# Kernel tuning notes

Measured on AMD Instinct MI355X. Metric: run time of the kernel, lower is better.

Reference implementation:

```python
import jax, jax.numpy as jnp
import numpy as np

C = 384        # channels
T_KERNEL = 121 # self.t, temporal kernel support
T_SIM = 65536  # simulated samples
SIZE = 2       # batch of simulations
BLOCK = 512    # overlap-add FFT block size (fast length >= T_KERNEL)


def _oa_conv_dewhiten(noise, spatial_std, vt_spatial, kernel_fft, s2):
    """Overlap-add FFT filtering (single_inv_oaconv1d, norm='ortho') then
    spatial dewhitening einsum, as in StationaryFactorizedNoise.simulate."""
    N, t_padded = noise.shape
    block_size = 2 * (kernel_fft.shape[0] - 1)
    t_out = t_padded - s2 + 1              # valid-conv output length
    hop = block_size - s2 + 1              # overlap-add segment length
    nb = -(-t_padded // hop)               # ceil division
    pad = nb * hop - t_padded
    x = jnp.pad(noise, ((0, 0), (0, pad))).reshape(N, nb, hop)
    xf = jnp.fft.rfft(x, n=block_size, axis=-1, norm='ortho')
    # kernel_fft is real (sqrt of mean power spectrum)
    yb = jnp.fft.irfft(xf * kernel_fft, n=block_size, axis=-1, norm='ortho')
    L = nb * hop + (block_size - hop)
    idx = (jnp.arange(nb)[:, None] * hop + jnp.arange(block_size)[None, :]).reshape(-1)
    y = jnp.zeros((N, L), noise.dtype).at[:, idx].add(yb.reshape(N, -1))
    y = y[:, s2 - 1: s2 - 1 + t_out]       # valid part of the convolution
    c = spatial_std.shape[0]
    noise3 = y.reshape(N // c, c, t_out)   # (size, c, t)
    spatial_part = spatial_std[:, None] * vt_spatial  # (c, d)
    return jnp.einsum('nct,cd->ntd', noise3, spatial_part)


def setup_inputs() -> dict:
    key = jax.random.key(0)
    k1, k2, k3, k4 = jax.random.split(key, 4)
    t_padded = T_SIM + T_KERNEL - 1
    return {
        'noise': jax.random.normal(k1, (SIZE * C, t_padded), dtype=jnp.float32),
        'spatial_std': jax.random.uniform(k2, (C,), dtype=jnp.float32, minval=0.5, maxval=1.5),
        'vt_spatial': jax.random.normal(k3, (C, C), dtype=jnp.float32) / np.sqrt(C),
        'kernel_fft': jax.random.uniform(k4, (BLOCK // 2 + 1,), dtype=jnp.float32, minval=0.1, maxval=1.0),
        's2': T_KERNEL,
    }


def reference(noise, spatial_std, vt_spatial, kernel_fft, s2):
    return _oa_conv_dewhiten(noise, spatial_std, vt_spatial, kernel_fft, s2)
```

## Files before the change

kernel.cpp:

```cpp
#include <hip/hip_runtime.h>
#include <hip/hip_bf16.h>

#define TPAD   65656
#define TOUT   65536
#define CCH    384
#define NROWS  768
#define HOP    392
#define NB     168
#define BS     512
#define KPAD   416
#define M1     129024
#define M2     131072

typedef __attribute__((ext_vector_type(8))) _Float16 f16x8;
typedef __attribute__((ext_vector_type(4))) _Float16 f16x4;
typedef __attribute__((ext_vector_type(4))) float    f32x4;
typedef __attribute__((ext_vector_type(8))) float    f32x8;

__device__ __forceinline__ void gload_lds16(const void* g, void* l) {
    __builtin_amdgcn_global_load_lds(
        (__attribute__((address_space(1))) void*)g,
        (__attribute__((address_space(3))) void*)l, 16, 0, 0);
}

__global__ void build_h_kernel(const float* __restrict__ kfft, float* __restrict__ h) {
    __shared__ float Ks[257];
    int j = threadIdx.x;
    if (j < 257) Ks[j] = kfft[j];
    __syncthreads();
    float acc = Ks[0] + ((j & 1) ? -Ks[256] : Ks[256]);
    const float w0 = 6.2831853071795864769f / 512.0f;
    for (int f = 1; f < 256; ++f) {
        int m = (f * j) & 511;
        acc += 2.0f * Ks[f] * cosf(w0 * (float)m);
    }
    h[j] = acc * (1.0f / 512.0f);
}

__global__ void build_ht_kernel(const float* __restrict__ h, _Float16* __restrict__ Ht) {
    int j = blockIdx.x;
    int i = blockIdx.y * 256 + threadIdx.x;
    if (i >= KPAD) return;
    float v = (i < HOP) ? h[(j - i) & 511] : 0.0f;
    Ht[j * KPAD + i] = (_Float16)v;
}

__global__ void build_spt_kernel(const float* __restrict__ sstd, const float* __restrict__ vt,
                                 _Float16* __restrict__ spT) {
    int d = blockIdx.x;
    int c = threadIdx.x;
    spT[d * CCH + c] = (_Float16)(sstd[c] * vt[c * CCH + d]);
}

__global__ __launch_bounds__(256) void gemm1_kernel(const float* __restrict__ noise,
                                                    const _Float16* __restrict__ Ht,
                                                    _Float16* __restrict__ yb) {
    __shared__ __align__(16) _Float16 As[128 * 32];
    __shared__ __align__(16) _Float16 Bs[128 * 32];
    const int tid  = threadIdx.x;
    const int lane = tid & 63;
    const int w    = tid >> 6;
    const int quad = lane >> 4, lm = lane & 15;
    const int wm   = w >> 1, wn = w & 1;

    const int bid = blockIdx.x + (blockIdx.y << 2);
    const int lid = (bid & 7) * 504 + (bid >> 3);
    const int n0  = (lid & 3) * 128;
    const int m0  = (lid >> 2) * 128;

    const int colseg = (tid & 3) * 8;
    const int arow0  = tid >> 2;
    const float* asrc0; const float* asrc1;
    int alim0, alim1;
    {
        int m = m0 + arow0;
        int r = m / NB, b = m - r * NB;
        asrc0 = noise + (size_t)r * TPAD + b * HOP;
        alim0 = (b == NB - 1) ? (TPAD - (NB - 1) * HOP) : HOP;
        m = m0 + arow0 + 64;
        r = m / NB; b = m - r * NB;
        asrc1 = noise + (size_t)r * TPAD + b * HOP;
        alim1 = (b == NB - 1) ? (TPAD - (NB - 1) * HOP) : HOP;
    }

    f32x4 pv00, pv01, pv10, pv11;
#define LOADA(K0) {                                                           \
        int i0 = (K0) + colseg;                                               \
        if (i0 < alim0) { pv00 = *(const f32x4*)(asrc0 + i0);                 \
                          pv01 = *(const f32x4*)(asrc0 + i0 + 4); }           \
        else            { pv00 = (f32x4){}; pv01 = (f32x4){}; }               \
        if (i0 < alim1) { pv10 = *(const f32x4*)(asrc1 + i0);                 \
                          pv11 = *(const f32x4*)(asrc1 + i0 + 4); }           \
        else            { pv10 = (f32x4){}; pv11 = (f32x4){}; }               \
    }

    LOADA(0);

    f32x4 acc[4][4] = {};

    for (int kt = 0; kt < KPAD / 32; ++kt) {
        const int k0 = kt * 32;
        gload_lds16(Ht + (n0 + arow0) * KPAD + k0 + colseg,
                    Bs + (tid & ~63) * 8);
        gload_lds16(Ht + (n0 + arow0 + 64) * KPAD + k0 + colseg,
                    Bs + (256 + (tid & ~63)) * 8);
        {
            f32x8 v0 = {pv00.x, pv00.y, pv00.z, pv00.w, pv01.x, pv01.y, pv01.z, pv01.w};
            *(f16x8*)(As + arow0 * 32 + colseg) = __builtin_convertvector(v0, f16x8);
            f32x8 v1 = {pv10.x, pv10.y, pv10.z, pv10.w, pv11.x, pv11.y, pv11.z, pv11.w};
            *(f16x8*)(As + (arow0 + 64) * 32 + colseg) = __builtin_convertvector(v1, f16x8);
        }
        __syncthreads();
        if (kt + 1 < KPAD / 32) { LOADA(k0 + 32); }

        f16x8 a[4], b[4];
#pragma unroll
        for (int mi = 0; mi < 4; ++mi)
            a[mi] = *(const f16x8*)(As + (wm * 64 + mi * 16 + lm) * 32 + quad * 8);
#pragma unroll
        for (int ni = 0; ni < 4; ++ni)
            b[ni] = *(const f16x8*)(Bs + (wn * 64 + ni * 16 + lm) * 32 + quad * 8);
#pragma unroll
        for (int mi = 0; mi < 4; ++mi)
#pragma unroll
            for (int ni = 0; ni < 4; ++ni)
                acc[mi][ni] = __builtin_amdgcn_mfma_f32_16x16x32_f16(a[mi], b[ni], acc[mi][ni], 0, 0, 0);
        __syncthreads();
    }
#undef LOADA

#pragma unroll
    for (int mi = 0; mi < 4; ++mi)
#pragma unroll
        for (int e = 0; e < 4; ++e) {
            int row = m0 + wm * 64 + mi * 16 + quad * 4 + e;
            f16x4 o = {(_Float16)acc[mi][0][e], (_Float16)acc[mi][1][e],
                       (_Float16)acc[mi][2][e], (_Float16)acc[mi][3][e]};
            *(f16x4*)(yb + (size_t)row * BS + n0 + wn * 64 + lm * 4) = o;
        }
}

__device__ __forceinline__ int permcol(int j) {
    return (j & ~63) | ((j & 15) << 2) | ((j >> 4) & 3);
}

__global__ __launch_bounds__(256) void oa_kernel(const _Float16* __restrict__ yb,
                                                 _Float16* __restrict__ Yt) {
    __shared__ float Ls[32][33];
    const int tx = threadIdx.x & 31, ty = threadIdx.x >> 5;
    const int t0 = blockIdx.x * 32, c0 = blockIdx.y * 32, n = blockIdx.z;
#pragma unroll
    for (int s = 0; s < 4; ++s) {
        int cc = ty + s * 8;
        int r  = n * CCH + c0 + cc;
        int g  = t0 + tx + 120;
        int b  = g / HOP;
        int j  = g - b * HOP;
        size_t base = (size_t)(r * NB + b) * BS;
        float v = (float)yb[base + permcol(j)];
        if (j < 120) v += (float)yb[base - BS + permcol(j + 392)];
        Ls[cc][tx] = v;
    }
    __syncthreads();
#pragma unroll
    for (int s = 0; s < 4; ++s) {
        int tt = ty + s * 8;
        Yt[((size_t)n * TOUT + t0 + tt) * CCH + c0 + tx] = (_Float16)Ls[tx][tt];
    }
}

__global__ __launch_bounds__(256) void gemm2_kernel(const _Float16* __restrict__ Yt,
                                                    const _Float16* __restrict__ spT,
                                                    float* __restrict__ outp) {
    __shared__ __align__(16) _Float16 As[128 * 32];
    __shared__ __align__(16) _Float16 Bs[128 * 32];
    const int tid  = threadIdx.x;
    const int w    = tid >> 6, lane = tid & 63;
    const int quad = lane >> 4, lm = lane & 15;
    const int wm   = w >> 1, wn = w & 1;

    const int bid = blockIdx.x + blockIdx.y * 3;
    const int lid = (bid & 7) * 384 + (bid >> 3);
    const int n0  = (lid % 3) * 128;
    const int m0  = (lid / 3) * 128;

    f32x4 acc[4][4] = {};

    for (int kt = 0; kt < CCH / 32; ++kt) {
        const int k0 = kt * 32;
#pragma unroll
        for (int ro = 0; ro < 2; ++ro) {
            int gidx = ro * 256 + tid;
            int row  = gidx >> 2;
            int col  = (gidx & 3) * 8;
            gload_lds16(Yt + (size_t)(m0 + row) * CCH + k0 + col,
                        As + (ro * 256 + (tid & ~63)) * 8);
            gload_lds16(spT + (n0 + row) * CCH + k0 + col,
                        Bs + (ro * 256 + (tid & ~63)) * 8);
        }
        __syncthreads();

        f16x8 a[4], b[4];
#pragma unroll
        for (int mi = 0; mi < 4; ++mi)
            a[mi] = *(const f16x8*)(As + (wm * 64 + mi * 16 + lm) * 32 + quad * 8);
#pragma unroll
        for (int ni = 0; ni < 4; ++ni)
            b[ni] = *(const f16x8*)(Bs + (wn * 64 + ni * 16 + lm) * 32 + quad * 8);
#pragma unroll
        for (int mi = 0; mi < 4; ++mi)
#pragma unroll
            for (int ni = 0; ni < 4; ++ni)
                acc[mi][ni] = __builtin_amdgcn_mfma_f32_16x16x32_f16(a[mi], b[ni], acc[mi][ni], 0, 0, 0);
        __syncthreads();
    }

#pragma unroll
    for (int mi = 0; mi < 4; ++mi)
#pragma unroll
        for (int e = 0; e < 4; ++e) {
            int row = m0 + wm * 64 + mi * 16 + quad * 4 + e;
            float* dst = outp + (size_t)row * CCH + n0 + wn * 64 + lm;
#pragma unroll
            for (int ni = 0; ni < 4; ++ni)
                dst[ni * 16] = acc[mi][ni][e];
        }
}

extern "C" void kernel_launch(void* const* d_in, const int* in_sizes, int n_in,
                              void* d_out, int out_size, void* d_ws, size_t ws_size,
                              hipStream_t stream) {
    const float* noise = (const float*)d_in[0];
    const float* sstd  = (const float*)d_in[1];
    const float* vt    = (const float*)d_in[2];
    const float* kfft  = (const float*)d_in[3];
    float* out = (float*)d_out;

    char* ws = (char*)d_ws;
    float*    h   = (float*)ws;
    _Float16* Ht  = (_Float16*)(ws + 2048);
    _Float16* spT = (_Float16*)(ws + 428032);
    _Float16* yb  = (_Float16*)(ws + 722944);
    _Float16* Yt  = (_Float16*)(ws + 132843520);

    build_h_kernel  <<<1, 512, 0, stream>>>(kfft, h);
    build_ht_kernel <<<dim3(512, 2), 256, 0, stream>>>(h, Ht);
    build_spt_kernel<<<CCH, CCH, 0, stream>>>(sstd, vt, spT);

    gemm1_kernel<<<dim3(BS / 128, M1 / 128), 256, 0, stream>>>(noise, Ht, yb);
    oa_kernel   <<<dim3(TOUT / 32, CCH / 32, 2), 256, 0, stream>>>(yb, Yt);
    gemm2_kernel<<<dim3(CCH / 128, M2 / 128), 256, 0, stream>>>(Yt, spT, out);
}
```

Measured before the change: 639.4 us.

## Double-buffer LDS tiles in the block-convolution GEMM to drop one barrier per step

```diff
diff --git a/kernel.cpp b/kernel.cpp
--- a/kernel.cpp
+++ b/kernel.cpp
@@ -11,6 +11,7 @@
 #define KPAD   416
 #define M1     129024
 #define M2     131072
+#define NT1    13
 
 typedef __attribute__((ext_vector_type(8))) _Float16 f16x8;
 typedef __attribute__((ext_vector_type(4))) _Float16 f16x4;
@@ -55,8 +56,8 @@
 __global__ __launch_bounds__(256) void gemm1_kernel(const float* __restrict__ noise,
                                                     const _Float16* __restrict__ Ht,
                                                     _Float16* __restrict__ yb) {
-    __shared__ __align__(16) _Float16 As[128 * 32];
-    __shared__ __align__(16) _Float16 Bs[128 * 32];
+    __shared__ __align__(16) _Float16 As[2][128 * 32];
+    __shared__ __align__(16) _Float16 Bs[2][128 * 32];
     const int tid  = threadIdx.x;
     const int lane = tid & 63;
     const int w    = tid >> 6;
@@ -93,33 +94,42 @@
                           pv11 = *(const f32x4*)(asrc1 + i0 + 4); }           \
         else            { pv10 = (f32x4){}; pv11 = (f32x4){}; }               \
     }
+#define CVTA(BUF) {                                                           \
+        f32x8 v0 = {pv00.x, pv00.y, pv00.z, pv00.w, pv01.x, pv01.y, pv01.z, pv01.w}; \
+        *(f16x8*)(&As[BUF][0] + arow0 * 32 + colseg) = __builtin_convertvector(v0, f16x8); \
+        f32x8 v1 = {pv10.x, pv10.y, pv10.z, pv10.w, pv11.x, pv11.y, pv11.z, pv11.w}; \
+        *(f16x8*)(&As[BUF][0] + (arow0 + 64) * 32 + colseg) = __builtin_convertvector(v1, f16x8); \
+    }
+#define LOADB(KT, BUF) {                                                      \
+        gload_lds16(Ht + (n0 + arow0) * KPAD + (KT) * 32 + colseg,            \
+                    &Bs[BUF][0] + (tid & ~63) * 8);                           \
+        gload_lds16(Ht + (n0 + arow0 + 64) * KPAD + (KT) * 32 + colseg,       \
+                    &Bs[BUF][0] + 256 * 8 + (tid & ~63) * 8);                 \
+    }
 
     LOADA(0);
+    LOADB(0, 0);
+    CVTA(0);
+    LOADA(32);
+    __syncthreads();
 
     f32x4 acc[4][4] = {};
 
-    for (int kt = 0; kt < KPAD / 32; ++kt) {
-        const int k0 = kt * 32;
-        gload_lds16(Ht + (n0 + arow0) * KPAD + k0 + colseg,
-                    Bs + (tid & ~63) * 8);
-        gload_lds16(Ht + (n0 + arow0 + 64) * KPAD + k0 + colseg,
-                    Bs + (256 + (tid & ~63)) * 8);
-        {
-            f32x8 v0 = {pv00.x, pv00.y, pv00.z, pv00.w, pv01.x, pv01.y, pv01.z, pv01.w};
-            *(f16x8*)(As + arow0 * 32 + colseg) = __builtin_convertvector(v0, f16x8);
-            f32x8 v1 = {pv10.x, pv10.y, pv10.z, pv10.w, pv11.x, pv11.y, pv11.z, pv11.w};
-            *(f16x8*)(As + (arow0 + 64) * 32 + colseg) = __builtin_convertvector(v1, f16x8);
-        }
-        __syncthreads();
-        if (kt + 1 < KPAD / 32) { LOADA(k0 + 32); }
+    for (int kt = 0; kt < NT1; ++kt) {
+        const int cur = kt & 1, nxt = cur ^ 1;
+        if (kt + 1 < NT1) {
+            LOADB(kt + 1, nxt);
+            CVTA(nxt);
+            if (kt + 2 < NT1) LOADA((kt + 2) * 32);
+        }
 
         f16x8 a[4], b[4];
 #pragma unroll
         for (int mi = 0; mi < 4; ++mi)
-            a[mi] = *(const f16x8*)(As + (wm * 64 + mi * 16 + lm) * 32 + quad * 8);
+            a[mi] = *(const f16x8*)(&As[cur][0] + (wm * 64 + mi * 16 + lm) * 32 + quad * 8);
 #pragma unroll
         for (int ni = 0; ni < 4; ++ni)
-            b[ni] = *(const f16x8*)(Bs + (wn * 64 + ni * 16 + lm) * 32 + quad * 8);
+            b[ni] = *(const f16x8*)(&Bs[cur][0] + (wn * 64 + ni * 16 + lm) * 32 + quad * 8);
 #pragma unroll
         for (int mi = 0; mi < 4; ++mi)
 #pragma unroll
@@ -128,6 +138,8 @@
         __syncthreads();
     }
 #undef LOADA
+#undef CVTA
+#undef LOADB
 
 #pragma unroll
     for (int mi = 0; mi < 4; ++mi)
```

After: 660.3 us. 3.3% more time.

## Restructure gemm1: preload full B slab to LDS, feed A from registers

Applied to the files above, without the earlier changes.

```diff
diff --git a/kernel.cpp b/kernel.cpp
--- a/kernel.cpp
+++ b/kernel.cpp
@@ -11,9 +11,11 @@
 #define KPAD   416
 #define M1     129024
 #define M2     131072
+#define NT1    13
 
 typedef __attribute__((ext_vector_type(8))) _Float16 f16x8;
 typedef __attribute__((ext_vector_type(4))) _Float16 f16x4;
+typedef __attribute__((ext_vector_type(2))) _Float16 f16x2;
 typedef __attribute__((ext_vector_type(4))) float    f32x4;
 typedef __attribute__((ext_vector_type(8))) float    f32x8;
 
@@ -55,77 +57,73 @@
 __global__ __launch_bounds__(256) void gemm1_kernel(const float* __restrict__ noise,
                                                     const _Float16* __restrict__ Ht,
                                                     _Float16* __restrict__ yb) {
-    __shared__ __align__(16) _Float16 As[128 * 32];
-    __shared__ __align__(16) _Float16 Bs[128 * 32];
+    __shared__ __align__(16) _Float16 Bs[NT1 * 64 * 32];
     const int tid  = threadIdx.x;
     const int lane = tid & 63;
     const int w    = tid >> 6;
     const int quad = lane >> 4, lm = lane & 15;
     const int wm   = w >> 1, wn = w & 1;
 
-    const int bid = blockIdx.x + (blockIdx.y << 2);
-    const int lid = (bid & 7) * 504 + (bid >> 3);
-    const int n0  = (lid & 3) * 128;
-    const int m0  = (lid >> 2) * 128;
-
-    const int colseg = (tid & 3) * 8;
-    const int arow0  = tid >> 2;
-    const float* asrc0; const float* asrc1;
-    int alim0, alim1;
+    const int bid = blockIdx.x;
+    const int lid = (bid & 7) * 1008 + (bid >> 3);
+    const int n0  = (lid & 7) * 64;
+    const int m0  = (lid >> 3) * 128;
+
     {
-        int m = m0 + arow0;
+        int row = tid >> 2, col = (tid & 3) * 8;
+        const _Float16* src = Ht + (n0 + row) * KPAD + col;
+        _Float16* dst = &Bs[0] + (tid & ~63) * 8;
+#pragma unroll
+        for (int kt = 0; kt < NT1; ++kt)
+            gload_lds16(src + kt * 32, dst + kt * 2048);
+    }
+
+    const float* asrc[4]; int alim[4];
+#pragma unroll
+    for (int mi = 0; mi < 4; ++mi) {
+        int m = m0 + wm * 64 + mi * 16 + lm;
         int r = m / NB, b = m - r * NB;
-        asrc0 = noise + (size_t)r * TPAD + b * HOP;
-        alim0 = (b == NB - 1) ? (TPAD - (NB - 1) * HOP) : HOP;
-        m = m0 + arow0 + 64;
-        r = m / NB; b = m - r * NB;
-        asrc1 = noise + (size_t)r * TPAD + b * HOP;
-        alim1 = (b == NB - 1) ? (TPAD - (NB - 1) * HOP) : HOP;
-    }
-
-    f32x4 pv00, pv01, pv10, pv11;
-#define LOADA(K0) {                                                           \
-        int i0 = (K0) + colseg;                                               \
-        if (i0 < alim0) { pv00 = *(const f32x4*)(asrc0 + i0);                 \
-                          pv01 = *(const f32x4*)(asrc0 + i0 + 4); }           \
-        else            { pv00 = (f32x4){}; pv01 = (f32x4){}; }               \
-        if (i0 < alim1) { pv10 = *(const f32x4*)(asrc1 + i0);                 \
-                          pv11 = *(const f32x4*)(asrc1 + i0 + 4); }           \
-        else            { pv10 = (f32x4){}; pv11 = (f32x4){}; }               \
+        asrc[mi] = noise + (size_t)r * TPAD + b * HOP;
+        alim[mi] = (b == NB - 1) ? (TPAD - (NB - 1) * HOP) : HOP;
+    }
+
+    f32x4 pv[4][2];
+#define LOADA(K0) {                                                        \
+        int i0 = (K0) + quad * 8;                                          \
+        _Pragma("unroll")                                                  \
+        for (int mi = 0; mi < 4; ++mi) {                                   \
+            if (i0 < alim[mi]) {                                           \
+                pv[mi][0] = *(const f32x4*)(asrc[mi] + i0);                \
+                pv[mi][1] = *(const f32x4*)(asrc[mi] + i0 + 4);            \
+            } else { pv[mi][0] = (f32x4){}; pv[mi][1] = (f32x4){}; }       \
+        }                                                                  \
     }
 
     LOADA(0);
-
-    f32x4 acc[4][4] = {};
-
-    for (int kt = 0; kt < KPAD / 32; ++kt) {
-        const int k0 = kt * 32;
-        gload_lds16(Ht + (n0 + arow0) * KPAD + k0 + colseg,
-                    Bs + (tid & ~63) * 8);
-        gload_lds16(Ht + (n0 + arow0 + 64) * KPAD + k0 + colseg,
-                    Bs + (256 + (tid & ~63)) * 8);
-        {
-            f32x8 v0 = {pv00.x, pv00.y, pv00.z, pv00.w, pv01.x, pv01.y, pv01.z, pv01.w};
-            *(f16x8*)(As + arow0 * 32 + colseg) = __builtin_convertvector(v0, f16x8);
-            f32x8 v1 = {pv10.x, pv10.y, pv10.z, pv10.w, pv11.x, pv11.y, pv11.z, pv11.w};
-            *(f16x8*)(As + (arow0 + 64) * 32 + colseg) = __builtin_convertvector(v1, f16x8);
-        }
-        __syncthreads();
-        if (kt + 1 < KPAD / 32) { LOADA(k0 + 32); }
-
-        f16x8 a[4], b[4];
+    __syncthreads();
+
+    f32x4 acc[4][2] = {};
+
+    for (int kt = 0; kt < NT1; ++kt) {
+        f16x8 a[4];
+#pragma unroll
+        for (int mi = 0; mi < 4; ++mi) {
+            f32x8 v = {pv[mi][0].x, pv[mi][0].y, pv[mi][0].z, pv[mi][0].w,
+                       pv[mi][1].x, pv[mi][1].y, pv[mi][1].z, pv[mi][1].w};
+            a[mi] = __builtin_convertvector(v, f16x8);
+        }
+        if (kt + 1 < NT1) LOADA((kt + 1) * 32);
+
+        f16x8 b[2];
+#pragma unroll
+        for (int ni = 0; ni < 2; ++ni)
+            b[ni] = *(const f16x8*)(&Bs[0] + kt * 2048 +
+                                    (wn * 32 + ni * 16 + lm) * 32 + quad * 8);
 #pragma unroll
         for (int mi = 0; mi < 4; ++mi)
-            a[mi] = *(const f16x8*)(As + (wm * 64 + mi * 16 + lm) * 32 + quad * 8);
-#pragma unroll
-        for (int ni = 0; ni < 4; ++ni)
-            b[ni] = *(const f16x8*)(Bs + (wn * 64 + ni * 16 + lm) * 32 + quad * 8);
-#pragma unroll
-        for (int mi = 0; mi < 4; ++mi)
-#pragma unroll
-            for (int ni = 0; ni < 4; ++ni)
+#pragma unroll
+            for (int ni = 0; ni < 2; ++ni)
                 acc[mi][ni] = __builtin_amdgcn_mfma_f32_16x16x32_f16(a[mi], b[ni], acc[mi][ni], 0, 0, 0);
-        __syncthreads();
     }
 #undef LOADA
 
@@ -134,14 +132,13 @@
 #pragma unroll
         for (int e = 0; e < 4; ++e) {
             int row = m0 + wm * 64 + mi * 16 + quad * 4 + e;
-            f16x4 o = {(_Float16)acc[mi][0][e], (_Float16)acc[mi][1][e],
-                       (_Float16)acc[mi][2][e], (_Float16)acc[mi][3][e]};
-            *(f16x4*)(yb + (size_t)row * BS + n0 + wn * 64 + lm * 4) = o;
+            f16x2 o = {(_Float16)acc[mi][0][e], (_Float16)acc[mi][1][e]};
+            *(f16x2*)(yb + (size_t)row * BS + n0 + wn * 32 + lm * 2) = o;
         }
 }
 
 __device__ __forceinline__ int permcol(int j) {
-    return (j & ~63) | ((j & 15) << 2) | ((j >> 4) & 3);
+    return (j & ~31) | ((j & 15) << 1) | ((j >> 4) & 1);
 }
 
 __global__ __launch_bounds__(256) void oa_kernel(const _Float16* __restrict__ yb,
@@ -247,7 +244,7 @@
     build_ht_kernel <<<dim3(512, 2), 256, 0, stream>>>(h, Ht);
     build_spt_kernel<<<CCH, CCH, 0, stream>>>(sstd, vt, spT);
 
-    gemm1_kernel<<<dim3(BS / 128, M1 / 128), 256, 0, stream>>>(noise, Ht, yb);
+    gemm1_kernel<<<M1 / 128 * (BS / 64), 256, 0, stream>>>(noise, Ht, yb);
     oa_kernel   <<<dim3(TOUT / 32, CCH / 32, 2), 256, 0, stream>>>(yb, Yt);
     gemm2_kernel<<<dim3(CCH / 128, M2 / 128), 256, 0, stream>>>(Yt, spT, out);
 }
```

Result: slower. 805.0 us (+25.9%).

## Stream fp32 noise tiles directly into LDS in gemm1, with a padded tail buffer

Applied to the files above, without the earlier changes.

```diff
diff --git a/kernel.cpp b/kernel.cpp
--- a/kernel.cpp
+++ b/kernel.cpp
@@ -11,6 +11,8 @@
 #define KPAD   416
 #define M1     129024
 #define M2     131072
+#define NT1    13
+#define TAIL   192
 
 typedef __attribute__((ext_vector_type(8))) _Float16 f16x8;
 typedef __attribute__((ext_vector_type(4))) _Float16 f16x4;
@@ -52,10 +54,19 @@
     spT[d * CCH + c] = (_Float16)(sstd[c] * vt[c * CCH + d]);
 }
 
+__global__ void build_fix_kernel(const float* __restrict__ noise, float* __restrict__ fixA) {
+    int r = blockIdx.x;
+    for (int i = threadIdx.x; i < KPAD; i += 256) {
+        float v = (i < TAIL) ? noise[(size_t)r * TPAD + (size_t)(NB - 1) * HOP + i] : 0.0f;
+        fixA[r * KPAD + i] = v;
+    }
+}
+
 __global__ __launch_bounds__(256) void gemm1_kernel(const float* __restrict__ noise,
+                                                    const float* __restrict__ fixA,
                                                     const _Float16* __restrict__ Ht,
                                                     _Float16* __restrict__ yb) {
-    __shared__ __align__(16) _Float16 As[128 * 32];
+    __shared__ __align__(16) float    As[128 * 32];
     __shared__ __align__(16) _Float16 Bs[128 * 32];
     const int tid  = threadIdx.x;
     const int lane = tid & 63;
@@ -68,55 +79,45 @@
     const int n0  = (lid & 3) * 128;
     const int m0  = (lid >> 2) * 128;
 
-    const int colseg = (tid & 3) * 8;
-    const int arow0  = tid >> 2;
-    const float* asrc0; const float* asrc1;
-    int alim0, alim1;
-    {
-        int m = m0 + arow0;
-        int r = m / NB, b = m - r * NB;
-        asrc0 = noise + (size_t)r * TPAD + b * HOP;
-        alim0 = (b == NB - 1) ? (TPAD - (NB - 1) * HOP) : HOP;
-        m = m0 + arow0 + 64;
-        r = m / NB; b = m - r * NB;
-        asrc1 = noise + (size_t)r * TPAD + b * HOP;
-        alim1 = (b == NB - 1) ? (TPAD - (NB - 1) * HOP) : HOP;
-    }
-
-    f32x4 pv00, pv01, pv10, pv11;
-#define LOADA(K0) {                                                           \
-        int i0 = (K0) + colseg;                                               \
-        if (i0 < alim0) { pv00 = *(const f32x4*)(asrc0 + i0);                 \
-                          pv01 = *(const f32x4*)(asrc0 + i0 + 4); }           \
-        else            { pv00 = (f32x4){}; pv01 = (f32x4){}; }               \
-        if (i0 < alim1) { pv10 = *(const f32x4*)(asrc1 + i0);                 \
-                          pv11 = *(const f32x4*)(asrc1 + i0 + 4); }           \
-        else            { pv10 = (f32x4){}; pv11 = (f32x4){}; }               \
-    }
-
-    LOADA(0);
+    const float* asrc[4];
+#pragma unroll
+    for (int ro = 0; ro < 4; ++ro) {
+        int s   = ro * 256 + tid;
+        int row = s >> 3;
+        int m   = m0 + row;
+        int r   = m / NB, b = m - r * NB;
+        const float* base = (b == NB - 1) ? (fixA + (size_t)r * KPAD)
+                                          : (noise + (size_t)r * TPAD + b * HOP);
+        asrc[ro] = base + (s & 7) * 4;
+    }
+    const _Float16* bsrc[2];
+#pragma unroll
+    for (int ro = 0; ro < 2; ++ro) {
+        int s = ro * 256 + tid;
+        bsrc[ro] = Ht + (n0 + (s >> 2)) * KPAD + (s & 3) * 8;
+    }
 
     f32x4 acc[4][4] = {};
 
-    for (int kt = 0; kt < KPAD / 32; ++kt) {
+    for (int kt = 0; kt < NT1; ++kt) {
         const int k0 = kt * 32;
-        gload_lds16(Ht + (n0 + arow0) * KPAD + k0 + colseg,
-                    Bs + (tid & ~63) * 8);
-        gload_lds16(Ht + (n0 + arow0 + 64) * KPAD + k0 + colseg,
-                    Bs + (256 + (tid & ~63)) * 8);
-        {
-            f32x8 v0 = {pv00.x, pv00.y, pv00.z, pv00.w, pv01.x, pv01.y, pv01.z, pv01.w};
-            *(f16x8*)(As + arow0 * 32 + colseg) = __builtin_convertvector(v0, f16x8);
-            f32x8 v1 = {pv10.x, pv10.y, pv10.z, pv10.w, pv11.x, pv11.y, pv11.z, pv11.w};
-            *(f16x8*)(As + (arow0 + 64) * 32 + colseg) = __builtin_convertvector(v1, f16x8);
-        }
-        __syncthreads();
-        if (kt + 1 < KPAD / 32) { LOADA(k0 + 32); }
+#pragma unroll
+        for (int ro = 0; ro < 4; ++ro)
+            gload_lds16(asrc[ro] + k0, As + (ro * 256 + (tid & ~63)) * 4);
+#pragma unroll
+        for (int ro = 0; ro < 2; ++ro)
+            gload_lds16(bsrc[ro] + k0, Bs + (ro * 256 + (tid & ~63)) * 8);
+        __syncthreads();
 
         f16x8 a[4], b[4];
 #pragma unroll
-        for (int mi = 0; mi < 4; ++mi)
-            a[mi] = *(const f16x8*)(As + (wm * 64 + mi * 16 + lm) * 32 + quad * 8);
+        for (int mi = 0; mi < 4; ++mi) {
+            const float* p = As + (wm * 64 + mi * 16 + lm) * 32 + quad * 8;
+            f32x4 v0 = *(const f32x4*)p;
+            f32x4 v1 = *(const f32x4*)(p + 4);
+            f32x8 v  = {v0.x, v0.y, v0.z, v0.w, v1.x, v1.y, v1.z, v1.w};
+            a[mi] = __builtin_convertvector(v, f16x8);
+        }
 #pragma unroll
         for (int ni = 0; ni < 4; ++ni)
             b[ni] = *(const f16x8*)(Bs + (wn * 64 + ni * 16 + lm) * 32 + quad * 8);
@@ -127,7 +128,6 @@
                 acc[mi][ni] = __builtin_amdgcn_mfma_f32_16x16x32_f16(a[mi], b[ni], acc[mi][ni], 0, 0, 0);
         __syncthreads();
     }
-#undef LOADA
 
 #pragma unroll
     for (int mi = 0; mi < 4; ++mi)
@@ -237,17 +237,19 @@
     float* out = (float*)d_out;
 
     char* ws = (char*)d_ws;
-    float*    h   = (float*)ws;
-    _Float16* Ht  = (_Float16*)(ws + 2048);
-    _Float16* spT = (_Float16*)(ws + 428032);
-    _Float16* yb  = (_Float16*)(ws + 722944);
-    _Float16* Yt  = (_Float16*)(ws + 132843520);
+    float*    h    = (float*)ws;
+    _Float16* Ht   = (_Float16*)(ws + 2048);
+    _Float16* spT  = (_Float16*)(ws + 428032);
+    _Float16* yb   = (_Float16*)(ws + 722944);
+    _Float16* Yt   = (_Float16*)(ws + 132843520);
+    float*    fixA = (float*)(ws + 233506816);
 
     build_h_kernel  <<<1, 512, 0, stream>>>(kfft, h);
     build_ht_kernel <<<dim3(512, 2), 256, 0, stream>>>(h, Ht);
     build_spt_kernel<<<CCH, CCH, 0, stream>>>(sstd, vt, spT);
-
-    gemm1_kernel<<<dim3(BS / 128, M1 / 128), 256, 0, stream>>>(noise, Ht, yb);
+    build_fix_kernel<<<NROWS, 256, 0, stream>>>(noise, fixA);
+
+    gemm1_kernel<<<dim3(BS / 128, M1 / 128), 256, 0, stream>>>(noise, fixA, Ht, yb);
     oa_kernel   <<<dim3(TOUT / 32, CCH / 32, 2), 256, 0, stream>>>(yb, Yt);
     gemm2_kernel<<<dim3(CCH / 128, M2 / 128), 256, 0, stream>>>(Yt, spT, out);
 }
```

Measured after the change: 640.1 us. No clear change (+0.1%).
